# Performance work log

Measured on AMD Instinct MI355X. Metric: run time of the kernel, lower is better.

Reference implementation:

```python
import jax, jax.numpy as jnp
import numpy as np

N, C, H, W = 512, 64, 32, 32
HID, HEADS = 128, 4
E = 16384
BN_EPS = 1e-5


def conv2d(x, w, b, pad):
    y = jax.lax.conv_general_dilated(x, w, (1, 1), [(pad, pad), (pad, pad)],
                                     dimension_numbers=('NCHW', 'OIHW', 'NCHW'))
    return y + b[None, :, None, None]


def bn_eval(x, g, b):
    # inference BN with running_mean=0, running_var=1
    scale = g * (1.0 / np.sqrt(1.0 + BN_EPS))
    return x * scale[None, :, None, None] + b[None, :, None, None]


def gat_layer(x, src, dst, lin_w, att_s, att_d, bias):
    # x: (N, in) -> (N, HID); PyG GATConv heads=4, concat=False, add_self_loops
    h = (x @ lin_w).reshape(N, HEADS, HID)          # (N, H, D)
    a_s = jnp.einsum('nhd,hd->nh', h, att_s)        # source score
    a_d = jnp.einsum('nhd,hd->nh', h, att_d)        # target score
    e = jax.nn.leaky_relu(a_s[src] + a_d[dst], 0.2)  # (E', H)
    m = jax.ops.segment_max(e, dst, num_segments=N)
    ex = jnp.exp(e - m[dst])
    denom = jax.ops.segment_sum(ex, dst, num_segments=N)
    alpha = ex / (denom[dst] + 1e-16)               # per-target softmax
    out = jax.ops.segment_sum(alpha[:, :, None] * h[src], dst, num_segments=N)
    return out.mean(axis=1) + bias                  # concat=False -> head mean


def setup_inputs() -> dict:
    key = jax.random.key(0)
    ks = jax.random.split(key, 24)
    s = lambda *shape: 0.05
    d = {}
    d['x'] = jax.random.normal(ks[0], (N, C, H, W), jnp.float32)
    d['edge_index'] = jax.random.randint(ks[1], (2, E), 0, N, jnp.int64)
    d['confidence_maps'] = jax.random.uniform(ks[2], (N, 1, H, W), jnp.float32)
    # feature encoder: 1x1 conv + BN
    d['fe_w'] = jax.random.normal(ks[3], (HID, C, 1, 1), jnp.float32) * 0.05
    d['fe_b'] = jnp.zeros((HID,), jnp.float32)
    d['fe_g'] = jnp.ones((HID,), jnp.float32)
    d['fe_beta'] = jnp.zeros((HID,), jnp.float32)
    # spatial processor: two 3x3 conv + BN
    d['sp_w1'] = jax.random.normal(ks[4], (HID, HID, 3, 3), jnp.float32) * 0.02
    d['sp_b1'] = jnp.zeros((HID,), jnp.float32)
    d['sp_g1'] = jnp.ones((HID,), jnp.float32)
    d['sp_be1'] = jnp.zeros((HID,), jnp.float32)
    d['sp_w2'] = jax.random.normal(ks[5], (HID, HID, 3, 3), jnp.float32) * 0.02
    d['sp_b2'] = jnp.zeros((HID,), jnp.float32)
    d['sp_g2'] = jnp.ones((HID,), jnp.float32)
    d['sp_be2'] = jnp.zeros((HID,), jnp.float32)
    # GAT layers (in=HID, out=HID, heads=HEADS)
    d['g1_lin'] = jax.random.normal(ks[6], (HID, HEADS * HID), jnp.float32) * 0.05
    d['g1_as'] = jax.random.normal(ks[7], (HEADS, HID), jnp.float32) * 0.05
    d['g1_ad'] = jax.random.normal(ks[8], (HEADS, HID), jnp.float32) * 0.05
    d['g1_b'] = jnp.zeros((HID,), jnp.float32)
    d['g2_lin'] = jax.random.normal(ks[9], (HID, HEADS * HID), jnp.float32) * 0.05
    d['g2_as'] = jax.random.normal(ks[10], (HEADS, HID), jnp.float32) * 0.05
    d['g2_ad'] = jax.random.normal(ks[11], (HEADS, HID), jnp.float32) * 0.05
    d['g2_b'] = jnp.zeros((HID,), jnp.float32)
    # output projector 1x1 conv
    d['op_w'] = jax.random.normal(ks[12], (C, HID, 1, 1), jnp.float32) * 0.05
    d['op_b'] = jnp.zeros((C,), jnp.float32)
    return d


def reference(x, edge_index, confidence_maps, fe_w, fe_b, fe_g, fe_beta,
              sp_w1, sp_b1, sp_g1, sp_be1, sp_w2, sp_b2, sp_g2, sp_be2,
              g1_lin, g1_as, g1_ad, g1_b, g2_lin, g2_as, g2_ad, g2_b,
              op_w, op_b):
    # feature encoder + confidence modulation
    xe = jax.nn.relu(bn_eval(conv2d(x, fe_w, fe_b, 0), fe_g, fe_beta))
    xe = xe * confidence_maps
    # spatial processor
    xp = jax.nn.relu(bn_eval(conv2d(xe, sp_w1, sp_b1, 1), sp_g1, sp_be1))
    xp = jax.nn.relu(bn_eval(conv2d(xp, sp_w2, sp_b2, 1), sp_g2, sp_be2))
    # global avg pool -> node features (N, HID)
    x_node = xp.mean(axis=(2, 3))
    # add self loops once
    sl = jnp.arange(N, dtype=edge_index.dtype)
    src = jnp.concatenate([edge_index[0], sl])
    dst = jnp.concatenate([edge_index[1], sl])
    xg = jax.nn.relu(gat_layer(x_node, src, dst, g1_lin, g1_as, g1_ad, g1_b))
    xg = jax.nn.relu(gat_layer(xg, src, dst, g2_lin, g2_as, g2_ad, g2_b))
    # broadcast-add GNN output back onto spatial maps
    x_comb = xg[:, :, None, None] + xp
    return conv2d(x_comb, op_w, op_b, 0)
```

## Files before the change

### kernel.cpp

```cpp
#include <hip/hip_runtime.h>
#include <stdint.h>

#define NIMG 512
#define CINCH 64
#define HIDC 128
#define NEDGE 16384
#define HWPIX 1024
#define PW2 34
#define PPIX 1156
#define APITCH 144
#define AROW 4896

typedef __attribute__((ext_vector_type(8))) short bf16x8;
typedef __attribute__((ext_vector_type(4))) float f32x4;
typedef __attribute__((ext_vector_type(16))) float f32x16;

static __device__ __forceinline__ unsigned short f2bf(float f){
  unsigned u = __builtin_bit_cast(unsigned, f);
  u += 0x7FFFu + ((u>>16)&1u);
  return (unsigned short)(u>>16);
}
static __device__ __forceinline__ float bf2f(unsigned short s){
  unsigned u = ((unsigned)s)<<16;
  return __builtin_bit_cast(float, u);
}

static __device__ __forceinline__ void gload16(const char* src, char* dst){
  __builtin_amdgcn_global_load_lds(
      (const __attribute__((address_space(1))) unsigned int*)src,
      (__attribute__((address_space(3))) unsigned int*)dst, 16, 0, 0);
}

__global__ void k_init(unsigned short* xe_pad, unsigned short* xp1_pad,
                       float* xnode_acc, int* cnt, int* pos){
  int idx = blockIdx.x*256 + threadIdx.x;
  int total_b = NIMG*132*16;
  for(int i = idx; i < total_b; i += gridDim.x*256){
    int img = i / (132*16);
    int rem = i - img*(132*16);
    int bp = rem >> 4;
    int slot = rem & 15;
    int r, c;
    if(bp < 34){ r = 0; c = bp; }
    else if(bp < 68){ r = 33; c = bp-34; }
    else if(bp < 100){ r = bp-68+1; c = 0; }
    else { r = bp-100+1; c = 33; }
    size_t off = ((size_t)img*PPIX + r*PW2 + c)*128 + slot*8;
    uint4 z = {0,0,0,0};
    *(uint4*)(xe_pad + off) = z;
    *(uint4*)(xp1_pad + off) = z;
  }
  for(int i = idx; i < NIMG*HIDC; i += gridDim.x*256) xnode_acc[i] = 0.f;
  for(int i = idx; i < NIMG; i += gridDim.x*256){ cnt[i] = 0; pos[i] = 0; }
}

__global__ void k_wconv(const float* __restrict__ sp_w1, const float* __restrict__ sp_w2,
                        const float* __restrict__ fe_w, const float* __restrict__ op_w,
                        unsigned short* Wb1, unsigned short* Wb2,
                        unsigned short* Wfe, unsigned short* Wop){
  int idx = blockIdx.x*256 + threadIdx.x;
  for(int i = idx; i < 147456; i += gridDim.x*256){
    int j = i & 7, pos = (i>>3)&7, co = (i>>6)&127, img = i>>13;
    int h = img/9, tap = img - 9*h;
    int cin = h*64 + (((pos - 3*co) & 7)<<3) + j;
    Wb1[i] = f2bf(sp_w1[(co*128+cin)*9 + tap]);
    Wb2[i] = f2bf(sp_w2[(co*128+cin)*9 + tap]);
  }
  for(int i = idx; i < 8192; i += gridDim.x*256){
    int j = i & 7, s = (i>>3)&7, co = i>>6;
    int ci = ((s ^ (co&7))<<3) + j;
    Wfe[i] = f2bf(fe_w[co*64+ci]);
  }
  for(int i = idx; i < 8192; i += gridDim.x*256){
    int j = i & 7, s = (i>>3)&15, co = i>>7;
    int cin = ((s ^ (co&7))<<3) + j;
    Wop[i] = f2bf(op_w[co*128+cin]);
  }
}

__global__ void k_csr_count(const int* __restrict__ ei, int* cnt){
  int e = blockIdx.x*256 + threadIdx.x;
  if(e < NEDGE) atomicAdd(&cnt[ei[NEDGE+e]], 1);
}
__global__ void k_csr_scan(const int* __restrict__ cnt, int* offs){
  __shared__ int sc[512];
  int t = threadIdx.x;
  sc[t] = cnt[t] + 1;
  __syncthreads();
  for(int o = 1; o < 512; o <<= 1){
    int add = (t >= o) ? sc[t-o] : 0;
    __syncthreads();
    sc[t] += add;
    __syncthreads();
  }
  if(t == 0) offs[0] = 0;
  offs[t+1] = sc[t];
}
__global__ void k_csr_fill(const int* __restrict__ ei, const int* __restrict__ offs,
                           int* pos, int* csr_src){
  int e = blockIdx.x*256 + threadIdx.x;
  if(e < NEDGE + NIMG){
    int s, d;
    if(e < NEDGE){ s = ei[e]; d = ei[NEDGE+e]; }
    else { s = e - NEDGE; d = s; }
    int slot = offs[d] + atomicAdd(&pos[d], 1);
    csr_src[slot] = s;
  }
}

__launch_bounds__(256, 2)
__global__ void k_encode(const float* __restrict__ x, const float* __restrict__ conf,
                         const unsigned short* __restrict__ Wfe,
                         const float* __restrict__ fe_b, const float* __restrict__ fe_g,
                         const float* __restrict__ fe_beta,
                         unsigned short* __restrict__ xe_pad){
  __shared__ char lds[49152];
  char* xa = lds; char* wb = lds + 32768;
  int tid = threadIdx.x;
  int n = blockIdx.x >> 3, rg = blockIdx.x & 7;
  int hw0 = rg*128;
  {
    int q = tid >> 3, c0 = tid & 7;
    const float* xb = x + (size_t)n*CINCH*HWPIX + hw0;
    #pragma unroll
    for(int cc = 0; cc < 8; ++cc){
      int c = cc*8 + c0;
      float4 v = *(const float4*)(xb + (size_t)c*HWPIX + q*4);
      float vv[4] = {v.x, v.y, v.z, v.w};
      #pragma unroll
      for(int i = 0; i < 4; ++i){
        int p = q*4 + i;
        *(float*)(xa + p*256 + ((cc ^ (p&7))*32) + c0*4) = vv[i];
      }
    }
    #pragma unroll
    for(int it = 0; it < 4; ++it){
      uint4 w = *(const uint4*)((const char*)Wfe + it*4096 + tid*16);
      *(uint4*)(wb + it*4096 + tid*16) = w;
    }
  }
  __syncthreads();
  int wid = tid>>6, lane = tid&63;
  int wr = wid>>1, wc = wid&1, fr = lane&15, fq = lane>>4;
  f32x4 acc[4][4];
  #pragma unroll
  for(int a = 0; a < 4; ++a)
    #pragma unroll
    for(int b = 0; b < 4; ++b) acc[a][b] = (f32x4){0.f,0.f,0.f,0.f};
  #pragma unroll
  for(int kc = 0; kc < 2; ++kc){
    bf16x8 af[4], bfr[4];
    #pragma unroll
    for(int mi = 0; mi < 4; ++mi){
      int p = wr*64 + mi*16 + fr;
      int u = kc*4 + fq;
      const float* src = (const float*)(xa + p*256 + ((u ^ (p&7))*32));
      float4 lo = *(const float4*)src;
      float4 hi = *(const float4*)(src+4);
      bf16x8 a;
      a[0]=(short)f2bf(lo.x); a[1]=(short)f2bf(lo.y); a[2]=(short)f2bf(lo.z); a[3]=(short)f2bf(lo.w);
      a[4]=(short)f2bf(hi.x); a[5]=(short)f2bf(hi.y); a[6]=(short)f2bf(hi.z); a[7]=(short)f2bf(hi.w);
      af[mi] = a;
    }
    #pragma unroll
    for(int nf = 0; nf < 4; ++nf){
      int co = wc*64 + nf*16 + fr;
      int slot = (kc*4 + fq) ^ (co&7);
      bfr[nf] = *(const bf16x8*)(wb + co*128 + slot*16);
    }
    #pragma unroll
    for(int mi = 0; mi < 4; ++mi)
      #pragma unroll
      for(int nf = 0; nf < 4; ++nf)
        acc[mi][nf] = __builtin_amdgcn_mfma_f32_16x16x32_bf16(af[mi], bfr[nf], acc[mi][nf], 0,0,0);
  }
  __syncthreads();
  {
    const float rs = 0.9999950000374997f;
    float kb[4], ks[4], kbe[4];
    #pragma unroll
    for(int nf = 0; nf < 4; ++nf){
      int co = wc*64 + nf*16 + fr;
      kb[nf] = fe_b[co]; ks[nf] = fe_g[co]*rs; kbe[nf] = fe_beta[co];
    }
    #pragma unroll
    for(int mi = 0; mi < 4; ++mi)
      #pragma unroll
      for(int j = 0; j < 4; ++j){
        int px = wr*64 + mi*16 + fq*4 + j;
        float cf = conf[(size_t)n*HWPIX + hw0 + px];
        #pragma unroll
        for(int nf = 0; nf < 4; ++nf){
          float v = (acc[mi][nf][j] + kb[nf])*ks[nf] + kbe[nf];
          v = fmaxf(v, 0.f)*cf;
          int co = wc*64 + nf*16 + fr;
          *(unsigned short*)(xa + px*256 + ((co*2) ^ (((px>>2)&7)<<4))) = f2bf(v);
        }
      }
  }
  __syncthreads();
  {
    int p = tid>>1, half = tid&1;
    int r = rg*4 + (p>>5), c = p&31;
    int key = 2*((p&31) + 1);
    unsigned short* dst = xe_pad + ((size_t)n*PPIX + (r+1)*PW2 + (c+1))*128;
    #pragma unroll
    for(int s = 0; s < 8; ++s){
      int ls = half*8 + s;
      uint4 v = *(uint4*)(xa + p*256 + ((ls*16) ^ (((p>>2)&7)<<4)));
      int pos = (ls>>3)*8 + (((ls&7) + key)&7);
      *(uint4*)(dst + pos*8) = v;
    }
  }
}

__launch_bounds__(256, 2)
__global__ void k_conv3(const unsigned short* __restrict__ inp,
                        const unsigned short* __restrict__ Wb,
                        const float* __restrict__ bnb, const float* __restrict__ bng,
                        const float* __restrict__ bnbe,
                        unsigned short* __restrict__ outp,
                        float* __restrict__ xnode_acc, int mode){
  extern __shared__ char lds[];
  char* Ab = lds;
  char* Wd = lds + 49152;
  int tid = threadIdx.x;
  int n = blockIdx.x>>2, rg = blockIdx.x&3;

  const char* img  = (const char*)inp + ((size_t)n*PPIX + (size_t)rg*8*PW2)*256;
  const char* wsrc = (const char*)Wb;

  #pragma unroll
  for(int it = 0; it < 4; ++it)
    gload16(wsrc + it*4096 + tid*16, Wd + it*4096 + tid*16);
  #pragma unroll
  for(int it = 0; it < 12; ++it){
    int j = tid + it*256;
    int q9 = j/9;
    int s = j - 9*q9;
    int pidx = q9 > 339 ? 339 : q9;
    int ss = (s == 8) ? 0 : s;
    gload16(img + (size_t)pidx*256 + 0*128 + ss*16, Ab + (size_t)j*16);
  }

  int wid = tid>>6, lane = tid&63;
  int wr = wid>>1, wc = wid&1;
  int col = lane&31, hi = lane>>5;
  int cob = (wc*64 + col)*128;

  f32x16 acc[4][2];
  #pragma unroll
  for(int a = 0; a < 4; ++a)
    #pragma unroll
    for(int b = 0; b < 2; ++b)
      #pragma unroll
      for(int r = 0; r < 16; ++r) acc[a][b][r] = 0.f;

  __syncthreads();

  for(int h = 0; h < 2; ++h){
    if(h == 1){
      #pragma unroll
      for(int it = 0; it < 12; ++it){
        int j = tid + it*256;
        int q9 = j/9;
        int s = j - 9*q9;
        int pidx = q9 > 339 ? 339 : q9;
        int ss = (s == 8) ? 0 : s;
        gload16(img + (size_t)pidx*256 + 128 + ss*16, Ab + (size_t)j*16);
      }
      __syncthreads();
    }
    for(int tap = 0; tap < 9; ++tap){
      int q = h*9 + tap;
      if(q < 17){
        const char* ws = wsrc + (size_t)(q+1)*16384;
        char* wdst = Wd + ((q+1)&1)*16384;
        #pragma unroll
        for(int it = 0; it < 4; ++it)
          gload16(ws + it*4096 + tid*16, wdst + it*4096 + tid*16);
      }
      const char* cur = Wd + (q&1)*16384;
      int dy = tap/3 - 1, dx = tap - (tap/3)*3 - 1;
      int pcol = col + 1 + dx;
      int prow0 = wr*4 + 1 + dy;
      int a0b = (prow0*34 + pcol)*APITCH;
      int ka = 2*pcol;
      __builtin_amdgcn_s_setprio(1);
      #pragma unroll
      for(int kc = 0; kc < 4; ++kc){
        int g = kc*2 + hi;
        int sa = ((g + ka)&7)<<4;
        bf16x8 af0 = *(const bf16x8*)(Ab + a0b + sa);
        bf16x8 af1 = *(const bf16x8*)(Ab + a0b + AROW + sa);
        bf16x8 af2 = *(const bf16x8*)(Ab + a0b + 2*AROW + sa);
        bf16x8 af3 = *(const bf16x8*)(Ab + a0b + 3*AROW + sa);
        int sw = ((g + 3*col)&7)<<4;
        bf16x8 wf0 = *(const bf16x8*)(cur + cob + sw);
        bf16x8 wf1 = *(const bf16x8*)(cur + cob + 4096 + sw);
        acc[0][0] = __builtin_amdgcn_mfma_f32_32x32x16_bf16(af0, wf0, acc[0][0], 0,0,0);
        acc[0][1] = __builtin_amdgcn_mfma_f32_32x32x16_bf16(af0, wf1, acc[0][1], 0,0,0);
        acc[1][0] = __builtin_amdgcn_mfma_f32_32x32x16_bf16(af1, wf0, acc[1][0], 0,0,0);
        acc[1][1] = __builtin_amdgcn_mfma_f32_32x32x16_bf16(af1, wf1, acc[1][1], 0,0,0);
        acc[2][0] = __builtin_amdgcn_mfma_f32_32x32x16_bf16(af2, wf0, acc[2][0], 0,0,0);
        acc[2][1] = __builtin_amdgcn_mfma_f32_32x32x16_bf16(af2, wf1, acc[2][1], 0,0,0);
        acc[3][0] = __builtin_amdgcn_mfma_f32_32x32x16_bf16(af3, wf0, acc[3][0], 0,0,0);
        acc[3][1] = __builtin_amdgcn_mfma_f32_32x32x16_bf16(af3, wf1, acc[3][1], 0,0,0);
      }
      __builtin_amdgcn_s_setprio(0);
      __syncthreads();
    }
  }

  char* eb = lds;
  float sn0 = 0.f, sn1 = 0.f;
  {
    const float rs = 0.9999950000374997f;
    float kb[2], ks[2], kbe[2];
    #pragma unroll
    for(int nf = 0; nf < 2; ++nf){
      int co = wc*64 + nf*32 + col;
      kb[nf] = bnb[co]; ks[nf] = bng[co]*rs; kbe[nf] = bnbe[co];
    }
    #pragma unroll
    for(int mi = 0; mi < 4; ++mi)
      #pragma unroll
      for(int reg = 0; reg < 16; ++reg){
        int pc = (reg&3) + 8*(reg>>2) + 4*hi;
        int px = (wr*4 + mi)*32 + pc;
        #pragma unroll
        for(int nf = 0; nf < 2; ++nf){
          float v = (acc[mi][nf][reg] + kb[nf])*ks[nf] + kbe[nf];
          v = fmaxf(v, 0.f);
          if(nf == 0) sn0 += v; else sn1 += v;
          int co = wc*64 + nf*32 + col;
          *(unsigned short*)(eb + px*256 + ((co*2) ^ (((px>>2)&7)<<4))) = f2bf(v);
        }
      }
  }
  if(mode == 1){
    sn0 += __shfl_down(sn0, 32);
    sn1 += __shfl_down(sn1, 32);
    if(lane < 32){
      atomicAdd(&xnode_acc[n*HIDC + wc*64 + col], sn0);
      atomicAdd(&xnode_acc[n*HIDC + wc*64 + 32 + col], sn1);
    }
  }
  __syncthreads();
  {
    int half = tid&1;
    #pragma unroll
    for(int pb = 0; pb < 2; ++pb){
      int p = (tid>>1) + pb*128;
      int r = rg*8 + (p>>5), c = p&31;
      unsigned short* dst;
      int key;
      if(mode == 0){
        key = 2*((p&31) + 1);
        dst = outp + ((size_t)n*PPIX + (r+1)*PW2 + (c+1))*128;
      } else {
        key = 3*p;
        dst = outp + ((size_t)n*HWPIX + rg*256 + p)*128;
      }
      #pragma unroll
      for(int s = 0; s < 8; ++s){
        int ls = half*8 + s;
        uint4 v = *(uint4*)(eb + p*256 + ((ls*16) ^ (((p>>2)&7)<<4)));
        int pos = (ls>>3)*8 + (((ls&7) + key)&7);
        *(uint4*)(dst + pos*8) = v;
      }
    }
  }
}

__global__ void k_gat_lin(const float* __restrict__ xin, float scale,
                          const float* __restrict__ lin,
                          const float* __restrict__ as_, const float* __restrict__ ad_,
                          float* __restrict__ h, float* __restrict__ a_s, float* __restrict__ a_d){
  __shared__ float xs[128];
  __shared__ float rs0[4], rs1[4], rd0[4], rd1[4];
  int n = blockIdx.x, t = threadIdx.x;
  if(t < 128) xs[t] = xin[n*128 + t]*scale;
  __syncthreads();
  float o0 = 0.f, o1 = 0.f;
  for(int k = 0; k < 128; ++k){
    float xv = xs[k];
    o0 += xv*lin[k*512 + t];
    o1 += xv*lin[k*512 + t + 256];
  }
  h[(size_t)n*512 + t] = o0;
  h[(size_t)n*512 + t + 256] = o1;
  float s0 = o0*as_[t], s1 = o1*as_[t+256];
  float d0 = o0*ad_[t], d1 = o1*ad_[t+256];
  #pragma unroll
  for(int o = 32; o; o >>= 1){
    s0 += __shfl_down(s0, o); s1 += __shfl_down(s1, o);
    d0 += __shfl_down(d0, o); d1 += __shfl_down(d1, o);
  }
  int w = t>>6;
  if((t&63) == 0){ rs0[w]=s0; rs1[w]=s1; rd0[w]=d0; rd1[w]=d1; }
  __syncthreads();
  if(t < 4){
    if(t < 2){
      a_s[n*4+t] = rs0[2*t] + rs0[2*t+1];
      a_d[n*4+t] = rd0[2*t] + rd0[2*t+1];
    } else {
      a_s[n*4+t] = rs1[2*(t-2)] + rs1[2*(t-2)+1];
      a_d[n*4+t] = rd1[2*(t-2)] + rd1[2*(t-2)+1];
    }
  }
}

__global__ void k_gat_aggr(const int* __restrict__ offs, const int* __restrict__ csr_src,
                           const float* __restrict__ a_s, const float* __restrict__ a_d,
                           const float* __restrict__ h, const float* __restrict__ bias,
                           float* __restrict__ y){
  __shared__ int ssrc[2048];
  __shared__ float sex[4][2048];
  __shared__ float out4[512];
  __shared__ float adn[4], smax[4], sden[4];
  __shared__ float wred[4][4];
  int n = blockIdx.x, t = threadIdx.x;
  int base = offs[n], deg = offs[n+1] - base;
  if(t < 4) adn[t] = a_d[n*4 + t];
  __syncthreads();
  bool cached = (deg <= 2048);
  float lm0=-1e30f, lm1=-1e30f, lm2=-1e30f, lm3=-1e30f;
  for(int e = t; e < deg; e += 256){
    int s = csr_src[base + e];
    float v0 = a_s[s*4+0] + adn[0]; v0 = v0 > 0.f ? v0 : 0.2f*v0;
    float v1 = a_s[s*4+1] + adn[1]; v1 = v1 > 0.f ? v1 : 0.2f*v1;
    float v2 = a_s[s*4+2] + adn[2]; v2 = v2 > 0.f ? v2 : 0.2f*v2;
    float v3 = a_s[s*4+3] + adn[3]; v3 = v3 > 0.f ? v3 : 0.2f*v3;
    if(cached){ ssrc[e]=s; sex[0][e]=v0; sex[1][e]=v1; sex[2][e]=v2; sex[3][e]=v3; }
    lm0 = fmaxf(lm0, v0); lm1 = fmaxf(lm1, v1); lm2 = fmaxf(lm2, v2); lm3 = fmaxf(lm3, v3);
  }
  #pragma unroll
  for(int o = 32; o; o >>= 1){
    lm0 = fmaxf(lm0, __shfl_down(lm0, o)); lm1 = fmaxf(lm1, __shfl_down(lm1, o));
    lm2 = fmaxf(lm2, __shfl_down(lm2, o)); lm3 = fmaxf(lm3, __shfl_down(lm3, o));
  }
  int w = t>>6;
  if((t&63) == 0){ wred[w][0]=lm0; wred[w][1]=lm1; wred[w][2]=lm2; wred[w][3]=lm3; }
  __syncthreads();
  if(t < 4) smax[t] = fmaxf(fmaxf(wred[0][t], wred[1][t]), fmaxf(wred[2][t], wred[3][t]));
  __syncthreads();
  float m0 = smax[0], m1 = smax[1], m2 = smax[2], m3 = smax[3];
  float ls0=0.f, ls1=0.f, ls2=0.f, ls3=0.f;
  for(int e = t; e < deg; e += 256){
    float e0, e1, e2, e3;
    if(cached){ e0 = sex[0][e]; e1 = sex[1][e]; e2 = sex[2][e]; e3 = sex[3][e]; }
    else {
      int s = csr_src[base + e];
      e0 = a_s[s*4+0] + adn[0]; e0 = e0 > 0.f ? e0 : 0.2f*e0;
      e1 = a_s[s*4+1] + adn[1]; e1 = e1 > 0.f ? e1 : 0.2f*e1;
      e2 = a_s[s*4+2] + adn[2]; e2 = e2 > 0.f ? e2 : 0.2f*e2;
      e3 = a_s[s*4+3] + adn[3]; e3 = e3 > 0.f ? e3 : 0.2f*e3;
    }
    e0 = __expf(e0-m0); e1 = __expf(e1-m1); e2 = __expf(e2-m2); e3 = __expf(e3-m3);
    if(cached){ sex[0][e]=e0; sex[1][e]=e1; sex[2][e]=e2; sex[3][e]=e3; }
    ls0 += e0; ls1 += e1; ls2 += e2; ls3 += e3;
  }
  #pragma unroll
  for(int o = 32; o; o >>= 1){
    ls0 += __shfl_down(ls0, o); ls1 += __shfl_down(ls1, o);
    ls2 += __shfl_down(ls2, o); ls3 += __shfl_down(ls3, o);
  }
  __syncthreads();
  if((t&63) == 0){ wred[w][0]=ls0; wred[w][1]=ls1; wred[w][2]=ls2; wred[w][3]=ls3; }
  __syncthreads();
  if(t < 4) sden[t] = wred[0][t] + wred[1][t] + wred[2][t] + wred[3][t] + 1e-16f;
  __syncthreads();
  #pragma unroll
  for(int oo = 0; oo < 2; ++oo){
    int o = t + oo*256;
    int hd = o>>7, d = o&127;
    float mh = smax[hd];
    float accv = 0.f;
    for(int e = 0; e < deg; ++e){
      float ex; int s;
      if(cached){ ex = sex[hd][e]; s = ssrc[e]; }
      else {
        s = csr_src[base + e];
        float v = a_s[s*4+hd] + adn[hd]; v = v > 0.f ? v : 0.2f*v;
        ex = __expf(v - mh);
      }
      accv += ex * h[(size_t)s*512 + hd*128 + d];
    }
    out4[o] = accv / sden[hd];
  }
  __syncthreads();
  if(t < 128){
    float v = (out4[t] + out4[128+t] + out4[256+t] + out4[384+t])*0.25f + bias[t];
    y[n*128 + t] = fmaxf(v, 0.f);
  }
}

__global__ void k_nodebias(const float* __restrict__ xg2, const float* __restrict__ op_w,
                           const float* __restrict__ op_b, float* __restrict__ nb){
  int g = blockIdx.x*256 + threadIdx.x;
  if(g < NIMG*64){
    int n = g>>6, co = g&63;
    float acc = op_b[co];
    for(int k = 0; k < 128; ++k) acc += op_w[co*128+k]*xg2[n*128+k];
    nb[g] = acc;
  }
}

__launch_bounds__(256, 2)
__global__ void k_outconv(const unsigned short* __restrict__ xp2,
                          const unsigned short* __restrict__ Wop,
                          const float* __restrict__ nb, float* __restrict__ out){
  __shared__ char lds[16384];
  int tid = threadIdx.x;
  int n = blockIdx.x>>3, rg = blockIdx.x&7;
  #pragma unroll
  for(int it = 0; it < 4; ++it){
    uint4 v = *(const uint4*)((const char*)Wop + it*4096 + tid*16);
    *(uint4*)(lds + it*4096 + tid*16) = v;
  }
  __syncthreads();
  int wid = tid>>6, lane = tid&63;
  int wr = wid>>1, wc = wid&1, fr = lane&15, fq = lane>>4;
  f32x4 acc[4][2];
  #pragma unroll
  for(int a = 0; a < 4; ++a){ acc[a][0] = (f32x4){0.f,0.f,0.f,0.f}; acc[a][1] = (f32x4){0.f,0.f,0.f,0.f}; }
  const unsigned short* abase = xp2 + ((size_t)n*HWPIX + rg*128)*128;
  #pragma unroll
  for(int kc = 0; kc < 4; ++kc){
    bf16x8 af[4], bfr[2];
    #pragma unroll
    for(int mi = 0; mi < 4; ++mi){
      int p = wr*64 + mi*16 + fr;
      int G = kc*4 + fq;
      int pos = (G>>3)*8 + (((G&7) + 3*p)&7);
      af[mi] = *(const bf16x8*)(abase + p*128 + pos*8);
    }
    #pragma unroll
    for(int nf = 0; nf < 2; ++nf){
      int co = wc*32 + nf*16 + fr;
      int slot = (kc*4 + fq) ^ (co&7);
      bfr[nf] = *(const bf16x8*)(lds + co*256 + slot*16);
    }
    #pragma unroll
    for(int mi = 0; mi < 4; ++mi)
      #pragma unroll
      for(int nf = 0; nf < 2; ++nf)
        acc[mi][nf] = __builtin_amdgcn_mfma_f32_16x16x32_bf16(af[mi], bfr[nf], acc[mi][nf], 0,0,0);
  }
  #pragma unroll
  for(int mi = 0; mi < 4; ++mi)
    #pragma unroll
    for(int nf = 0; nf < 2; ++nf){
      int co = wc*32 + nf*16 + fr;
      int hw = rg*128 + wr*64 + mi*16 + fq*4;
      float nbv = nb[n*64 + co];
      float4 v = { acc[mi][nf][0]+nbv, acc[mi][nf][1]+nbv, acc[mi][nf][2]+nbv, acc[mi][nf][3]+nbv };
      *(float4*)(out + ((size_t)n*64 + co)*HWPIX + hw) = v;
    }
}

extern "C" void kernel_launch(void* const* d_in, const int* in_sizes, int n_in,
                              void* d_out, int out_size, void* d_ws, size_t ws_size,
                              hipStream_t stream){
  const float* x       = (const float*)d_in[0];
  const int*   ei      = (const int*)d_in[1];
  const float* conf    = (const float*)d_in[2];
  const float* fe_w    = (const float*)d_in[3];
  const float* fe_b    = (const float*)d_in[4];
  const float* fe_g    = (const float*)d_in[5];
  const float* fe_beta = (const float*)d_in[6];
  const float* sp_w1   = (const float*)d_in[7];
  const float* sp_b1   = (const float*)d_in[8];
  const float* sp_g1   = (const float*)d_in[9];
  const float* sp_be1  = (const float*)d_in[10];
  const float* sp_w2   = (const float*)d_in[11];
  const float* sp_b2   = (const float*)d_in[12];
  const float* sp_g2   = (const float*)d_in[13];
  const float* sp_be2  = (const float*)d_in[14];
  const float* g1_lin  = (const float*)d_in[15];
  const float* g1_as   = (const float*)d_in[16];
  const float* g1_ad   = (const float*)d_in[17];
  const float* g1_b    = (const float*)d_in[18];
  const float* g2_lin  = (const float*)d_in[19];
  const float* g2_as   = (const float*)d_in[20];
  const float* g2_ad   = (const float*)d_in[21];
  const float* g2_b    = (const float*)d_in[22];
  const float* op_w    = (const float*)d_in[23];
  const float* op_b    = (const float*)d_in[24];
  float* out = (float*)d_out;

  char* ws = (char*)d_ws;
  size_t off = 0;
  auto alloc = [&](size_t bytes)->char*{
    char* p = ws + off; off += (bytes + 255) & ~(size_t)255; return p;
  };
  unsigned short* bigA  = (unsigned short*)alloc((size_t)NIMG*PPIX*128*2);
  unsigned short* xp1   = (unsigned short*)alloc((size_t)NIMG*PPIX*128*2);
  unsigned short* Wb1   = (unsigned short*)alloc(147456*2);
  unsigned short* Wb2   = (unsigned short*)alloc(147456*2);
  unsigned short* Wfe   = (unsigned short*)alloc(8192*2);
  unsigned short* Wop   = (unsigned short*)alloc(8192*2);
  float* xnode_acc = (float*)alloc(NIMG*HIDC*4);
  float* h     = (float*)alloc((size_t)NIMG*512*4);
  float* a_s   = (float*)alloc(NIMG*4*4);
  float* a_d   = (float*)alloc(NIMG*4*4);
  float* xg1   = (float*)alloc(NIMG*HIDC*4);
  float* xg2   = (float*)alloc(NIMG*HIDC*4);
  int* cnt     = (int*)alloc(NIMG*4);
  int* pos     = (int*)alloc(NIMG*4);
  int* offs    = (int*)alloc((NIMG+1)*4);
  int* csr_src = (int*)alloc((NEDGE+NIMG)*4);
  float* nb    = (float*)alloc(NIMG*64*4);
  if(off > ws_size) return;
  unsigned short* xp2 = bigA;

  hipFuncSetAttribute((const void*)k_conv3,
                      hipFuncAttributeMaxDynamicSharedMemorySize, 81920);

  k_init<<<1024, 256, 0, stream>>>(bigA, xp1, xnode_acc, cnt, pos);
  k_wconv<<<576, 256, 0, stream>>>(sp_w1, sp_w2, fe_w, op_w, Wb1, Wb2, Wfe, Wop);
  k_csr_count<<<(NEDGE+255)/256, 256, 0, stream>>>(ei, cnt);
  k_csr_scan<<<1, 512, 0, stream>>>(cnt, offs);
  k_csr_fill<<<(NEDGE+NIMG+255)/256, 256, 0, stream>>>(ei, offs, pos, csr_src);
  k_encode<<<4096, 256, 0, stream>>>(x, conf, Wfe, fe_b, fe_g, fe_beta, bigA);
  k_conv3<<<2048, 256, 81920, stream>>>(bigA, Wb1, sp_b1, sp_g1, sp_be1, xp1, xnode_acc, 0);
  k_conv3<<<2048, 256, 81920, stream>>>(xp1, Wb2, sp_b2, sp_g2, sp_be2, xp2, xnode_acc, 1);
  k_gat_lin<<<512, 256, 0, stream>>>(xnode_acc, 1.f/1024.f, g1_lin, g1_as, g1_ad, h, a_s, a_d);
  k_gat_aggr<<<512, 256, 0, stream>>>(offs, csr_src, a_s, a_d, h, g1_b, xg1);
  k_gat_lin<<<512, 256, 0, stream>>>(xg1, 1.f, g2_lin, g2_as, g2_ad, h, a_s, a_d);
  k_gat_aggr<<<512, 256, 0, stream>>>(offs, csr_src, a_s, a_d, h, g2_b, xg2);
  k_nodebias<<<(NIMG*64+255)/256, 256, 0, stream>>>(xg2, op_w, op_b, nb);
  k_outconv<<<4096, 256, 0, stream>>>(xp2, Wop, nb, out);
}
```

Baseline: 544.7 us.

## Shrink conv3 tiles to 4 rows, read weights directly from global memory

The 3x3 conv kernel now splits each image into 8 row groups of 4 rows instead of 4 groups of 8, halving the per-wave accumulator tiles. It drops the double-buffered LDS weight staging and per-tap barriers, and instead loads weight fragments straight from global/L2 with an unswizzled weight layout. LDS drops to 32 KB and launch bounds allow 3 blocks per CU, aiming for higher occupancy and fewer syncs. In exchange, halo rows are reloaded more often and every wave re-reads weights from cache, which could make it memory bound.

```diff
diff --git a/kernel.cpp b/kernel.cpp
--- a/kernel.cpp
+++ b/kernel.cpp
@@ -60,9 +60,9 @@
                         unsigned short* Wfe, unsigned short* Wop){
   int idx = blockIdx.x*256 + threadIdx.x;
   for(int i = idx; i < 147456; i += gridDim.x*256){
-    int j = i & 7, pos = (i>>3)&7, co = (i>>6)&127, img = i>>13;
+    int j = i & 7, g = (i>>3)&7, co = (i>>6)&127, img = i>>13;
     int h = img/9, tap = img - 9*h;
-    int cin = h*64 + (((pos - 3*co) & 7)<<3) + j;
+    int cin = h*64 + g*8 + j;
     Wb1[i] = f2bf(sp_w1[(co*128+cin)*9 + tap]);
     Wb2[i] = f2bf(sp_w2[(co*128+cin)*9 + tap]);
   }
@@ -214,7 +214,7 @@
   }
 }
 
-__launch_bounds__(256, 2)
+__launch_bounds__(256, 3)
 __global__ void k_conv3(const unsigned short* __restrict__ inp,
                         const unsigned short* __restrict__ Wb,
                         const float* __restrict__ bnb, const float* __restrict__ bng,
@@ -223,94 +223,73 @@
                         float* __restrict__ xnode_acc, int mode){
   extern __shared__ char lds[];
   char* Ab = lds;
-  char* Wd = lds + 49152;
   int tid = threadIdx.x;
-  int n = blockIdx.x>>2, rg = blockIdx.x&3;
-
-  const char* img  = (const char*)inp + ((size_t)n*PPIX + (size_t)rg*8*PW2)*256;
+  int n = blockIdx.x>>3, rg = blockIdx.x&7;
+
+  const char* img  = (const char*)inp + ((size_t)n*PPIX + (size_t)rg*4*PW2)*256;
   const char* wsrc = (const char*)Wb;
-
-  #pragma unroll
-  for(int it = 0; it < 4; ++it)
-    gload16(wsrc + it*4096 + tid*16, Wd + it*4096 + tid*16);
-  #pragma unroll
-  for(int it = 0; it < 12; ++it){
-    int j = tid + it*256;
-    int q9 = j/9;
-    int s = j - 9*q9;
-    int pidx = q9 > 339 ? 339 : q9;
-    int ss = (s == 8) ? 0 : s;
-    gload16(img + (size_t)pidx*256 + 0*128 + ss*16, Ab + (size_t)j*16);
-  }
 
   int wid = tid>>6, lane = tid&63;
   int wr = wid>>1, wc = wid&1;
   int col = lane&31, hi = lane>>5;
-  int cob = (wc*64 + col)*128;
-
-  f32x16 acc[4][2];
-  #pragma unroll
-  for(int a = 0; a < 4; ++a)
+  const char* wlane = wsrc + (size_t)(wc*64 + col)*128 + hi*16;
+
+  f32x16 acc[2][2];
+  #pragma unroll
+  for(int a = 0; a < 2; ++a)
     #pragma unroll
     for(int b = 0; b < 2; ++b)
       #pragma unroll
       for(int r = 0; r < 16; ++r) acc[a][b][r] = 0.f;
 
+  #pragma unroll
+  for(int it = 0; it < 8; ++it){
+    int j = tid + it*256;
+    int q9 = j/9, s = j - 9*q9;
+    int pidx = q9 > 203 ? 203 : q9;
+    int ss = (s == 8) ? 0 : s;
+    gload16(img + (size_t)pidx*256 + ss*16, Ab + (size_t)j*16);
+  }
   __syncthreads();
 
   for(int h = 0; h < 2; ++h){
     if(h == 1){
-      #pragma unroll
-      for(int it = 0; it < 12; ++it){
+      __syncthreads();
+      #pragma unroll
+      for(int it = 0; it < 8; ++it){
         int j = tid + it*256;
-        int q9 = j/9;
-        int s = j - 9*q9;
-        int pidx = q9 > 339 ? 339 : q9;
+        int q9 = j/9, s = j - 9*q9;
+        int pidx = q9 > 203 ? 203 : q9;
         int ss = (s == 8) ? 0 : s;
         gload16(img + (size_t)pidx*256 + 128 + ss*16, Ab + (size_t)j*16);
       }
       __syncthreads();
     }
+    const char* wq = wlane + (size_t)h*9*16384;
+    #pragma unroll
     for(int tap = 0; tap < 9; ++tap){
-      int q = h*9 + tap;
-      if(q < 17){
-        const char* ws = wsrc + (size_t)(q+1)*16384;
-        char* wdst = Wd + ((q+1)&1)*16384;
-        #pragma unroll
-        for(int it = 0; it < 4; ++it)
-          gload16(ws + it*4096 + tid*16, wdst + it*4096 + tid*16);
-      }
-      const char* cur = Wd + (q&1)*16384;
+      const char* wt = wq + (size_t)tap*16384;
       int dy = tap/3 - 1, dx = tap - (tap/3)*3 - 1;
       int pcol = col + 1 + dx;
-      int prow0 = wr*4 + 1 + dy;
+      int prow0 = wr*2 + 1 + dy;
       int a0b = (prow0*34 + pcol)*APITCH;
       int ka = 2*pcol;
-      __builtin_amdgcn_s_setprio(1);
       #pragma unroll
       for(int kc = 0; kc < 4; ++kc){
         int g = kc*2 + hi;
         int sa = ((g + ka)&7)<<4;
         bf16x8 af0 = *(const bf16x8*)(Ab + a0b + sa);
         bf16x8 af1 = *(const bf16x8*)(Ab + a0b + AROW + sa);
-        bf16x8 af2 = *(const bf16x8*)(Ab + a0b + 2*AROW + sa);
-        bf16x8 af3 = *(const bf16x8*)(Ab + a0b + 3*AROW + sa);
-        int sw = ((g + 3*col)&7)<<4;
-        bf16x8 wf0 = *(const bf16x8*)(cur + cob + sw);
-        bf16x8 wf1 = *(const bf16x8*)(cur + cob + 4096 + sw);
+        bf16x8 wf0 = *(const bf16x8*)(wt + kc*32);
+        bf16x8 wf1 = *(const bf16x8*)(wt + 4096 + kc*32);
         acc[0][0] = __builtin_amdgcn_mfma_f32_32x32x16_bf16(af0, wf0, acc[0][0], 0,0,0);
         acc[0][1] = __builtin_amdgcn_mfma_f32_32x32x16_bf16(af0, wf1, acc[0][1], 0,0,0);
         acc[1][0] = __builtin_amdgcn_mfma_f32_32x32x16_bf16(af1, wf0, acc[1][0], 0,0,0);
         acc[1][1] = __builtin_amdgcn_mfma_f32_32x32x16_bf16(af1, wf1, acc[1][1], 0,0,0);
-        acc[2][0] = __builtin_amdgcn_mfma_f32_32x32x16_bf16(af2, wf0, acc[2][0], 0,0,0);
-        acc[2][1] = __builtin_amdgcn_mfma_f32_32x32x16_bf16(af2, wf1, acc[2][1], 0,0,0);
-        acc[3][0] = __builtin_amdgcn_mfma_f32_32x32x16_bf16(af3, wf0, acc[3][0], 0,0,0);
-        acc[3][1] = __builtin_amdgcn_mfma_f32_32x32x16_bf16(af3, wf1, acc[3][1], 0,0,0);
       }
-      __builtin_amdgcn_s_setprio(0);
-      __syncthreads();
-    }
-  }
+    }
+  }
+  __syncthreads();
 
   char* eb = lds;
   float sn0 = 0.f, sn1 = 0.f;
@@ -323,11 +302,11 @@
       kb[nf] = bnb[co]; ks[nf] = bng[co]*rs; kbe[nf] = bnbe[co];
     }
     #pragma unroll
-    for(int mi = 0; mi < 4; ++mi)
+    for(int mi = 0; mi < 2; ++mi)
       #pragma unroll
       for(int reg = 0; reg < 16; ++reg){
         int pc = (reg&3) + 8*(reg>>2) + 4*hi;
-        int px = (wr*4 + mi)*32 + pc;
+        int px = (wr*2 + mi)*32 + pc;
         #pragma unroll
         for(int nf = 0; nf < 2; ++nf){
           float v = (acc[mi][nf][reg] + kb[nf])*ks[nf] + kbe[nf];
@@ -348,27 +327,23 @@
   }
   __syncthreads();
   {
-    int half = tid&1;
-    #pragma unroll
-    for(int pb = 0; pb < 2; ++pb){
-      int p = (tid>>1) + pb*128;
-      int r = rg*8 + (p>>5), c = p&31;
-      unsigned short* dst;
-      int key;
-      if(mode == 0){
-        key = 2*((p&31) + 1);
-        dst = outp + ((size_t)n*PPIX + (r+1)*PW2 + (c+1))*128;
-      } else {
-        key = 3*p;
-        dst = outp + ((size_t)n*HWPIX + rg*256 + p)*128;
-      }
-      #pragma unroll
-      for(int s = 0; s < 8; ++s){
-        int ls = half*8 + s;
-        uint4 v = *(uint4*)(eb + p*256 + ((ls*16) ^ (((p>>2)&7)<<4)));
-        int pos = (ls>>3)*8 + (((ls&7) + key)&7);
-        *(uint4*)(dst + pos*8) = v;
-      }
+    int p = tid>>1, half = tid&1;
+    int r = rg*4 + (p>>5), c = p&31;
+    unsigned short* dst;
+    int key;
+    if(mode == 0){
+      key = 2*((p&31) + 1);
+      dst = outp + ((size_t)n*PPIX + (r+1)*PW2 + (c+1))*128;
+    } else {
+      key = 3*p;
+      dst = outp + ((size_t)n*HWPIX + rg*128 + p)*128;
+    }
+    #pragma unroll
+    for(int s = 0; s < 8; ++s){
+      int ls = half*8 + s;
+      uint4 v = *(uint4*)(eb + p*256 + ((ls*16) ^ (((p>>2)&7)<<4)));
+      int pos = (ls>>3)*8 + (((ls&7) + key)&7);
+      *(uint4*)(dst + pos*8) = v;
     }
   }
 }
@@ -616,7 +591,7 @@
   unsigned short* xp2 = bigA;
 
   hipFuncSetAttribute((const void*)k_conv3,
-                      hipFuncAttributeMaxDynamicSharedMemorySize, 81920);
+                      hipFuncAttributeMaxDynamicSharedMemorySize, 32768);
 
   k_init<<<1024, 256, 0, stream>>>(bigA, xp1, xnode_acc, cnt, pos);
   k_wconv<<<576, 256, 0, stream>>>(sp_w1, sp_w2, fe_w, op_w, Wb1, Wb2, Wfe, Wop);
@@ -624,8 +599,8 @@
   k_csr_scan<<<1, 512, 0, stream>>>(cnt, offs);
   k_csr_fill<<<(NEDGE+NIMG+255)/256, 256, 0, stream>>>(ei, offs, pos, csr_src);
   k_encode<<<4096, 256, 0, stream>>>(x, conf, Wfe, fe_b, fe_g, fe_beta, bigA);
-  k_conv3<<<2048, 256, 81920, stream>>>(bigA, Wb1, sp_b1, sp_g1, sp_be1, xp1, xnode_acc, 0);
-  k_conv3<<<2048, 256, 81920, stream>>>(xp1, Wb2, sp_b2, sp_g2, sp_be2, xp2, xnode_acc, 1);
+  k_conv3<<<4096, 256, 32768, stream>>>(bigA, Wb1, sp_b1, sp_g1, sp_be1, xp1, xnode_acc, 0);
+  k_conv3<<<4096, 256, 32768, stream>>>(xp1, Wb2, sp_b2, sp_g2, sp_be2, xp2, xnode_acc, 1);
   k_gat_lin<<<512, 256, 0, stream>>>(xnode_acc, 1.f/1024.f, g1_lin, g1_as, g1_ad, h, a_s, a_d);
   k_gat_aggr<<<512, 256, 0, stream>>>(offs, csr_src, a_s, a_d, h, g1_b, xg1);
   k_gat_lin<<<512, 256, 0, stream>>>(xg1, 1.f, g2_lin, g2_as, g2_ad, h, a_s, a_d);
```

New measurement: 911.9 us. 1.67x slower.
